# Performance work log

Measured on AMD Instinct MI355X. Metric: run time of the kernel, lower is better.

The kernel has to match this reference:

```python
import jax, jax.numpy as jnp
import numpy as np
from jax import lax

B, T_HIST, T_PRED = 8192, 11, 80
IN, H = 2, 64


def _glorot(key, shape, fan):
    bound = 1.0 / np.sqrt(fan)
    return jax.random.uniform(key, shape, jnp.float32, -bound, bound)


def setup_inputs() -> dict:
    key = jax.random.key(0)
    ks = jax.random.split(key, 20)
    inp = {"x": jax.random.normal(ks[0], (B, T_HIST, IN), jnp.float32)}
    # encoder / decoder: 2-layer tanh RNN, PyTorch param layout (out_features first)
    for pfx, base in (("enc", 1), ("dec", 9)):
        inp[f"{pfx}_Wih0"] = _glorot(ks[base + 0], (H, IN), H)
        inp[f"{pfx}_Whh0"] = _glorot(ks[base + 1], (H, H), H)
        inp[f"{pfx}_bih0"] = _glorot(ks[base + 2], (H,), H)
        inp[f"{pfx}_bhh0"] = _glorot(ks[base + 3], (H,), H)
        inp[f"{pfx}_Wih1"] = _glorot(ks[base + 4], (H, H), H)
        inp[f"{pfx}_Whh1"] = _glorot(ks[base + 5], (H, H), H)
        inp[f"{pfx}_bih1"] = _glorot(ks[base + 6], (H,), H)
        inp[f"{pfx}_bhh1"] = _glorot(ks[base + 7], (H,), H)
    inp["fc_W"] = _glorot(ks[17], (2, H), H)
    inp["fc_b"] = _glorot(ks[18], (2,), H)
    return inp


def _rnn_layer(x_seq, h0, Wih, Whh, bih, bhh):
    # x_seq: [T, B, in]; tanh RNN cell, returns (h_T, all hidden states [T, B, H])
    def step(h, x_t):
        h_new = jnp.tanh(x_t @ Wih.T + bih + h @ Whh.T + bhh)
        return h_new, h_new
    return lax.scan(step, h0, x_seq)


def reference(x,
              enc_Wih0, enc_Whh0, enc_bih0, enc_bhh0,
              enc_Wih1, enc_Whh1, enc_bih1, enc_bhh1,
              dec_Wih0, dec_Whh0, dec_bih0, dec_bhh0,
              dec_Wih1, dec_Whh1, dec_bih1, dec_bhh1,
              fc_W, fc_b):
    b = x.shape[0]
    h0 = jnp.zeros((b, H), x.dtype)
    x_seq = jnp.swapaxes(x, 0, 1)  # [T, B, 2]
    # encoder (dropout inactive in eval)
    h1_T, hs0 = _rnn_layer(x_seq, h0, enc_Wih0, enc_Whh0, enc_bih0, enc_bhh0)
    h2_T, _ = _rnn_layer(hs0, h0, enc_Wih1, enc_Whh1, enc_bih1, enc_bhh1)

    def dec_step(carry, _):
        h1, h2, inp = carry
        h1 = jnp.tanh(inp @ dec_Wih0.T + dec_bih0 + h1 @ dec_Whh0.T + dec_bhh0)
        h2 = jnp.tanh(h1 @ dec_Wih1.T + dec_bih1 + h2 @ dec_Whh1.T + dec_bhh1)
        pred = h2 @ fc_W.T + fc_b  # [B, 2]
        return (h1, h2, pred), pred

    init = (h1_T, h2_T, x[:, -1, :])
    _, preds = lax.scan(dec_step, init, None, length=T_PRED)  # [80, B, 2]
    return jnp.swapaxes(preds, 0, 1)  # [B, 80, 2]
```

## Files before the change

### kernel.cpp

```cpp
#include <hip/hip_runtime.h>

typedef __attribute__((ext_vector_type(8))) _Float16 f16x8;
typedef __attribute__((ext_vector_type(4))) float   f32x4;

namespace {
constexpr int kB    = 8192;
constexpr int kTH   = 11;
constexpr int kTP   = 80;
constexpr int kM    = 16;
constexpr int kStrH = 72;
}

__device__ __forceinline__ f16x8 cvt8(const float* f) {
    f16x8 v;
#pragma unroll
    for (int j = 0; j < 8; ++j) v[j] = (_Float16)f[j];
    return v;
}

__device__ __forceinline__ void loadB1(const float* __restrict__ W, int col, int q,
                                       f16x8 (&Bf)[2]) {
#pragma unroll
    for (int c = 0; c < 2; ++c) {
        const float* src = W + col * 64 + c * 32 + q * 8;
        const float4 a = reinterpret_cast<const float4*>(src)[0];
        const float4 b = reinterpret_cast<const float4*>(src)[1];
        float f[8] = {a.x, a.y, a.z, a.w, b.x, b.y, b.z, b.w};
        Bf[c] = cvt8(f);
    }
}

__device__ __forceinline__ void loadBfc(const float* __restrict__ fcW, int p, int q,
                                        f16x8 (&Bf)[2]) {
#pragma unroll
    for (int c = 0; c < 2; ++c) {
        float f[8];
#pragma unroll
        for (int j = 0; j < 8; ++j)
            f[j] = (p < 2) ? fcW[p * 64 + c * 32 + q * 8 + j] : 0.f;
        Bf[c] = cvt8(f);
    }
}

__device__ __forceinline__ void loadBG(const float* __restrict__ fcW, float w0, float w1,
                                       int q, f16x8 (&Bf)[2]) {
#pragma unroll
    for (int c = 0; c < 2; ++c) {
        float f[8];
#pragma unroll
        for (int j = 0; j < 8; ++j) {
            const int k = c * 32 + q * 8 + j;
            f[j] = w0 * fcW[k] + w1 * fcW[64 + k];
        }
        Bf[c] = cvt8(f);
    }
}

__device__ __forceinline__ f16x8 read_frag(const _Float16* plane, int off) {
    return *reinterpret_cast<const f16x8*>(plane + off);
}

__device__ __forceinline__ f32x4 mfma1(f16x8 a, f16x8 b, f32x4 acc) {
    return __builtin_amdgcn_mfma_f32_16x16x32_f16(a, b, acc, 0, 0, 0);
}

__device__ __forceinline__ float fast_tanh(float x) {
    const float e = __builtin_amdgcn_exp2f(x * 2.8853900817779268f);
    return fmaf(-2.0f, __builtin_amdgcn_rcpf(e + 1.0f), 1.0f);
}

__global__ __attribute__((amdgpu_waves_per_eu(2, 2))) __launch_bounds__(256)
void traj_rnn_kernel(
    const float* __restrict__ x,
    const float* __restrict__ eWih0, const float* __restrict__ eWhh0,
    const float* __restrict__ ebih0, const float* __restrict__ ebhh0,
    const float* __restrict__ eWih1, const float* __restrict__ eWhh1,
    const float* __restrict__ ebih1, const float* __restrict__ ebhh1,
    const float* __restrict__ dWih0, const float* __restrict__ dWhh0,
    const float* __restrict__ dbih0, const float* __restrict__ dbhh0,
    const float* __restrict__ dWih1, const float* __restrict__ dWhh1,
    const float* __restrict__ dbih1, const float* __restrict__ dbhh1,
    const float* __restrict__ fcW, const float* __restrict__ fcb,
    float* __restrict__ out)
{
    const int tid  = threadIdx.x;
    const int wv   = tid >> 6;
    const int lane = tid & 63;
    const int p    = lane & 15;
    const int q    = lane >> 4;
    const int col  = wv * 16 + p;
    const int r0   = blockIdx.x * kM;

    __shared__ __align__(16) _Float16 Hhi1[kM * kStrH];
    __shared__ __align__(16) _Float16 Hhi2[kM * kStrH];
    __shared__ __align__(16) float xbuf[kM * kTH * 2];
    __shared__ __align__(16) float predbuf[kM * kTP * 2];

    for (int i = tid; i < kM * kTH * 2; i += 256)
        xbuf[i] = x[r0 * (kTH * 2) + i];

    f16x8 H1f[2], H2f[2];
#pragma unroll
    for (int c = 0; c < 2; ++c) {
        H1f[c] = f16x8{0, 0, 0, 0, 0, 0, 0, 0};
        H2f[c] = f16x8{0, 0, 0, 0, 0, 0, 0, 0};
    }
    __syncthreads();

    const int aoff = p * kStrH;

    {
        const float b0 = ebih0[col] + ebhh0[col];
        const float b1 = ebih1[col] + ebhh1[col];
        const float w0 = eWih0[col * 2 + 0];
        const float w1 = eWih0[col * 2 + 1];
        f16x8 B0[2], B1[2], B2[2];
        loadB1(eWhh0, col, q, B0);
        loadB1(eWih1, col, q, B1);
        loadB1(eWhh1, col, q, B2);

        f32x4 P1 = {b0, b0, b0, b0};

#pragma unroll 1
        for (int t = 0; t < kTH; ++t) {
#pragma unroll
            for (int r = 0; r < 4; ++r) {
                const float2 xv = *reinterpret_cast<const float2*>(
                    &xbuf[(4 * q + r) * (kTH * 2) + 2 * t]);
                const float h1 = fast_tanh(fmaf(w0, xv.x, fmaf(w1, xv.y, P1[r])));
                Hhi1[(4 * q + r) * kStrH + col] = (_Float16)h1;
            }
            f32x4 a2 = {b1, b1, b1, b1};
#pragma unroll
            for (int c = 0; c < 2; ++c)
                a2 = mfma1(H2f[c], B2[c], a2);
            __syncthreads();

#pragma unroll
            for (int c = 0; c < 2; ++c)
                H1f[c] = read_frag(Hhi1, aoff + c * 32 + q * 8);
#pragma unroll
            for (int c = 0; c < 2; ++c)
                a2 = mfma1(H1f[c], B1[c], a2);
#pragma unroll
            for (int r = 0; r < 4; ++r) {
                const float h2 = fast_tanh(a2[r]);
                Hhi2[(4 * q + r) * kStrH + col] = (_Float16)h2;
            }
            __syncthreads();

#pragma unroll
            for (int c = 0; c < 2; ++c)
                H2f[c] = read_frag(Hhi2, aoff + c * 32 + q * 8);
            f32x4 np = {b0, b0, b0, b0};
#pragma unroll
            for (int c = 0; c < 2; ++c)
                np = mfma1(H1f[c], B0[c], np);
            P1 = np;
        }
    }

    {
        const float b0 = dbih0[col] + dbhh0[col];
        const float b1 = dbih1[col] + dbhh1[col];
        const float w0 = dWih0[col * 2 + 0];
        const float w1 = dWih0[col * 2 + 1];
        const float fb0 = fcb[0];
        const float fb1 = fcb[1];
        const float b0p = b0 + w0 * fb0 + w1 * fb1;
        const float fbp = (p == 0) ? fb0 : fb1;
        f16x8 B0[2], B1[2], B2[2], BF[2], BG[2];
        loadB1(dWhh0, col, q, B0);
        loadB1(dWih1, col, q, B1);
        loadB1(dWhh1, col, q, B2);
        loadBfc(fcW, p, q, BF);
        loadBG(fcW, w0, w1, q, BG);

        f32x4 P1 = {b0, b0, b0, b0};
#pragma unroll
        for (int c = 0; c < 2; ++c)
            P1 = mfma1(H1f[c], B0[c], P1);
#pragma unroll
        for (int r = 0; r < 4; ++r) {
            const float2 xv = *reinterpret_cast<const float2*>(
                &xbuf[(4 * q + r) * (kTH * 2) + 2 * (kTH - 1)]);
            P1[r] = fmaf(w0, xv.x, fmaf(w1, xv.y, P1[r]));
        }

#pragma unroll 2
        for (int t = 0; t < kTP; ++t) {
#pragma unroll
            for (int r = 0; r < 4; ++r) {
                const float h1 = fast_tanh(P1[r]);
                Hhi1[(4 * q + r) * kStrH + col] = (_Float16)h1;
            }
            f32x4 a2 = {b1, b1, b1, b1};
#pragma unroll
            for (int c = 0; c < 2; ++c)
                a2 = mfma1(H2f[c], B2[c], a2);
            __syncthreads();

#pragma unroll
            for (int c = 0; c < 2; ++c)
                H1f[c] = read_frag(Hhi1, aoff + c * 32 + q * 8);
#pragma unroll
            for (int c = 0; c < 2; ++c)
                a2 = mfma1(H1f[c], B1[c], a2);
#pragma unroll
            for (int r = 0; r < 4; ++r) {
                const float h2 = fast_tanh(a2[r]);
                Hhi2[(4 * q + r) * kStrH + col] = (_Float16)h2;
            }
            __syncthreads();

#pragma unroll
            for (int c = 0; c < 2; ++c)
                H2f[c] = read_frag(Hhi2, aoff + c * 32 + q * 8);
            f32x4 ng = {b0p, b0p, b0p, b0p};
            f32x4 nb = {0.f, 0.f, 0.f, 0.f};
#pragma unroll
            for (int c = 0; c < 2; ++c) {
                ng = mfma1(H2f[c], BG[c], ng);
                nb = mfma1(H1f[c], B0[c], nb);
            }
            P1 = ng + nb;

            f32x4 fcC = {0.f, 0.f, 0.f, 0.f};
#pragma unroll
            for (int c = 0; c < 2; ++c)
                fcC = mfma1(H2f[c], BF[c], fcC);
            if (wv == 0 && p < 2) {
#pragma unroll
                for (int r = 0; r < 4; ++r)
                    predbuf[((4 * q + r) * kTP + t) * 2 + p] = fcC[r] + fbp;
            }
        }
    }

    __syncthreads();
    {
        float4* dst = reinterpret_cast<float4*>(out + r0 * (kTP * 2));
        const float4* src = reinterpret_cast<const float4*>(predbuf);
        for (int i = tid; i < kM * kTP * 2 / 4; i += 256)
            dst[i] = src[i];
    }
}

extern "C" void kernel_launch(void* const* d_in, const int* in_sizes, int n_in,
                              void* d_out, int out_size, void* d_ws, size_t ws_size,
                              hipStream_t stream) {
    const float* x     = (const float*)d_in[0];
    const float* eWih0 = (const float*)d_in[1];
    const float* eWhh0 = (const float*)d_in[2];
    const float* ebih0 = (const float*)d_in[3];
    const float* ebhh0 = (const float*)d_in[4];
    const float* eWih1 = (const float*)d_in[5];
    const float* eWhh1 = (const float*)d_in[6];
    const float* ebih1 = (const float*)d_in[7];
    const float* ebhh1 = (const float*)d_in[8];
    const float* dWih0 = (const float*)d_in[9];
    const float* dWhh0 = (const float*)d_in[10];
    const float* dbih0 = (const float*)d_in[11];
    const float* dbhh0 = (const float*)d_in[12];
    const float* dWih1 = (const float*)d_in[13];
    const float* dWhh1 = (const float*)d_in[14];
    const float* dbih1 = (const float*)d_in[15];
    const float* dbhh1 = (const float*)d_in[16];
    const float* fcW   = (const float*)d_in[17];
    const float* fcb   = (const float*)d_in[18];
    float* out = (float*)d_out;

    dim3 grid(kB / kM);
    dim3 block(256);
    traj_rnn_kernel<<<grid, block, 0, stream>>>(
        x, eWih0, eWhh0, ebih0, ebhh0, eWih1, eWhh1, ebih1, ebhh1,
        dWih0, dWhh0, dbih0, dbhh0, dWih1, dWhh1, dbih1, dbhh1,
        fcW, fcb, out);
}
```

Measured before the change: 141.0 us.

## Ping-pong two 16-row groups per block to overlap recurrence phases

Each block now handles 32 rows in two groups of four waves. The groups run alternate halves of each RNN step (layer-1 phase vs layer-2 phase) between shared barriers, so one group's MFMA/tanh work fills the other's barrier wait. Weights for encoder and decoder are preloaded upfront, and the grid is halved with 512-thread blocks. This raises register pressure (both weight sets live) and couples the groups through block-wide barriers.

```diff
diff --git a/kernel.cpp b/kernel.cpp
--- a/kernel.cpp
+++ b/kernel.cpp
@@ -69,7 +69,7 @@
     return fmaf(-2.0f, __builtin_amdgcn_rcpf(e + 1.0f), 1.0f);
 }
 
-__global__ __attribute__((amdgpu_waves_per_eu(2, 2))) __launch_bounds__(256)
+__global__ __attribute__((amdgpu_waves_per_eu(2, 2))) __launch_bounds__(512)
 void traj_rnn_kernel(
     const float* __restrict__ x,
     const float* __restrict__ eWih0, const float* __restrict__ eWhh0,
@@ -84,164 +84,191 @@
     float* __restrict__ out)
 {
     const int tid  = threadIdx.x;
-    const int wv   = tid >> 6;
+    const int grp  = tid >> 8;
+    const int wvg  = (tid >> 6) & 3;
     const int lane = tid & 63;
     const int p    = lane & 15;
     const int q    = lane >> 4;
-    const int col  = wv * 16 + p;
-    const int r0   = blockIdx.x * kM;
-
-    __shared__ __align__(16) _Float16 Hhi1[kM * kStrH];
-    __shared__ __align__(16) _Float16 Hhi2[kM * kStrH];
-    __shared__ __align__(16) float xbuf[kM * kTH * 2];
-    __shared__ __align__(16) float predbuf[kM * kTP * 2];
-
-    for (int i = tid; i < kM * kTH * 2; i += 256)
-        xbuf[i] = x[r0 * (kTH * 2) + i];
-
-    f16x8 H1f[2], H2f[2];
-#pragma unroll
-    for (int c = 0; c < 2; ++c) {
-        H1f[c] = f16x8{0, 0, 0, 0, 0, 0, 0, 0};
-        H2f[c] = f16x8{0, 0, 0, 0, 0, 0, 0, 0};
-    }
-    __syncthreads();
-
+    const int col  = wvg * 16 + p;
+
+    __shared__ __align__(16) _Float16 H1s[2][kM * kStrH];
+    __shared__ __align__(16) _Float16 H2s[2][kM * kStrH];
+    __shared__ __align__(16) float xbuf[2][kM * kTH * 2];
+    __shared__ __align__(16) float predbuf[2][kM * kTP * 2];
+
+    for (int i = tid; i < 2 * kM * kTH * 2; i += 512)
+        (&xbuf[0][0])[i] = x[blockIdx.x * 32 * (kTH * 2) + i];
+
+    _Float16* h1p = H1s[grp];
+    _Float16* h2p = H2s[grp];
+    const float* xb = xbuf[grp];
+    float*       pb = predbuf[grp];
+
+    const f16x8 Z = {0, 0, 0, 0, 0, 0, 0, 0};
+    f16x8 H1f0 = Z, H1f1 = Z, H2f0 = Z, H2f1 = Z;
     const int aoff = p * kStrH;
 
-    {
-        const float b0 = ebih0[col] + ebhh0[col];
-        const float b1 = ebih1[col] + ebhh1[col];
-        const float w0 = eWih0[col * 2 + 0];
-        const float w1 = eWih0[col * 2 + 1];
-        f16x8 B0[2], B1[2], B2[2];
-        loadB1(eWhh0, col, q, B0);
-        loadB1(eWih1, col, q, B1);
-        loadB1(eWhh1, col, q, B2);
-
-        f32x4 P1 = {b0, b0, b0, b0};
-
-#pragma unroll 1
-        for (int t = 0; t < kTH; ++t) {
-#pragma unroll
-            for (int r = 0; r < 4; ++r) {
-                const float2 xv = *reinterpret_cast<const float2*>(
-                    &xbuf[(4 * q + r) * (kTH * 2) + 2 * t]);
-                const float h1 = fast_tanh(fmaf(w0, xv.x, fmaf(w1, xv.y, P1[r])));
-                Hhi1[(4 * q + r) * kStrH + col] = (_Float16)h1;
-            }
-            f32x4 a2 = {b1, b1, b1, b1};
-#pragma unroll
-            for (int c = 0; c < 2; ++c)
-                a2 = mfma1(H2f[c], B2[c], a2);
-            __syncthreads();
-
-#pragma unroll
-            for (int c = 0; c < 2; ++c)
-                H1f[c] = read_frag(Hhi1, aoff + c * 32 + q * 8);
-#pragma unroll
-            for (int c = 0; c < 2; ++c)
-                a2 = mfma1(H1f[c], B1[c], a2);
-#pragma unroll
-            for (int r = 0; r < 4; ++r) {
-                const float h2 = fast_tanh(a2[r]);
-                Hhi2[(4 * q + r) * kStrH + col] = (_Float16)h2;
-            }
-            __syncthreads();
-
-#pragma unroll
-            for (int c = 0; c < 2; ++c)
-                H2f[c] = read_frag(Hhi2, aoff + c * 32 + q * 8);
-            f32x4 np = {b0, b0, b0, b0};
-#pragma unroll
-            for (int c = 0; c < 2; ++c)
-                np = mfma1(H1f[c], B0[c], np);
-            P1 = np;
-        }
-    }
-
-    {
-        const float b0 = dbih0[col] + dbhh0[col];
-        const float b1 = dbih1[col] + dbhh1[col];
-        const float w0 = dWih0[col * 2 + 0];
-        const float w1 = dWih0[col * 2 + 1];
-        const float fb0 = fcb[0];
-        const float fb1 = fcb[1];
-        const float b0p = b0 + w0 * fb0 + w1 * fb1;
-        const float fbp = (p == 0) ? fb0 : fb1;
-        f16x8 B0[2], B1[2], B2[2], BF[2], BG[2];
-        loadB1(dWhh0, col, q, B0);
-        loadB1(dWih1, col, q, B1);
-        loadB1(dWhh1, col, q, B2);
-        loadBfc(fcW, p, q, BF);
-        loadBG(fcW, w0, w1, q, BG);
-
-        f32x4 P1 = {b0, b0, b0, b0};
-#pragma unroll
-        for (int c = 0; c < 2; ++c)
-            P1 = mfma1(H1f[c], B0[c], P1);
+    const float b0e = ebih0[col] + ebhh0[col];
+    const float b1e = ebih1[col] + ebhh1[col];
+    const float w0e = eWih0[col * 2 + 0];
+    const float w1e = eWih0[col * 2 + 1];
+    f16x8 B0e[2], B1e[2], B2e[2];
+    loadB1(eWhh0, col, q, B0e);
+    loadB1(eWih1, col, q, B1e);
+    loadB1(eWhh1, col, q, B2e);
+
+    const float b0d = dbih0[col] + dbhh0[col];
+    const float b1d = dbih1[col] + dbhh1[col];
+    const float w0d = dWih0[col * 2 + 0];
+    const float w1d = dWih0[col * 2 + 1];
+    const float fb0 = fcb[0];
+    const float fb1 = fcb[1];
+    const float b0p = b0d + w0d * fb0 + w1d * fb1;
+    const float fbp = (p == 0) ? fb0 : fb1;
+    f16x8 B0d[2], B1d[2], B2d[2], BG[2], BF[2];
+    loadB1(dWhh0, col, q, B0d);
+    loadB1(dWih1, col, q, B1d);
+    loadB1(dWhh1, col, q, B2d);
+    loadBG(fcW, w0d, w1d, q, BG);
+    loadBfc(fcW, p, q, BF);
+
+    f32x4 P1 = {b0e, b0e, b0e, b0e};
+    f32x4 a2 = {0.f, 0.f, 0.f, 0.f};
+    f32x4 nb = {0.f, 0.f, 0.f, 0.f};
+
+    __syncthreads();
+
+    auto A_enc = [&](int t) {
+        if (t > 0) {
+            H2f0 = read_frag(h2p, aoff + q * 8);
+            H2f1 = read_frag(h2p, aoff + 32 + q * 8);
+        }
 #pragma unroll
         for (int r = 0; r < 4; ++r) {
             const float2 xv = *reinterpret_cast<const float2*>(
-                &xbuf[(4 * q + r) * (kTH * 2) + 2 * (kTH - 1)]);
-            P1[r] = fmaf(w0, xv.x, fmaf(w1, xv.y, P1[r]));
-        }
-
-#pragma unroll 2
-        for (int t = 0; t < kTP; ++t) {
-#pragma unroll
-            for (int r = 0; r < 4; ++r) {
-                const float h1 = fast_tanh(P1[r]);
-                Hhi1[(4 * q + r) * kStrH + col] = (_Float16)h1;
-            }
-            f32x4 a2 = {b1, b1, b1, b1};
-#pragma unroll
-            for (int c = 0; c < 2; ++c)
-                a2 = mfma1(H2f[c], B2[c], a2);
-            __syncthreads();
-
-#pragma unroll
-            for (int c = 0; c < 2; ++c)
-                H1f[c] = read_frag(Hhi1, aoff + c * 32 + q * 8);
-#pragma unroll
-            for (int c = 0; c < 2; ++c)
-                a2 = mfma1(H1f[c], B1[c], a2);
-#pragma unroll
-            for (int r = 0; r < 4; ++r) {
-                const float h2 = fast_tanh(a2[r]);
-                Hhi2[(4 * q + r) * kStrH + col] = (_Float16)h2;
-            }
-            __syncthreads();
-
-#pragma unroll
-            for (int c = 0; c < 2; ++c)
-                H2f[c] = read_frag(Hhi2, aoff + c * 32 + q * 8);
-            f32x4 ng = {b0p, b0p, b0p, b0p};
-            f32x4 nb = {0.f, 0.f, 0.f, 0.f};
-#pragma unroll
-            for (int c = 0; c < 2; ++c) {
-                ng = mfma1(H2f[c], BG[c], ng);
-                nb = mfma1(H1f[c], B0[c], nb);
-            }
-            P1 = ng + nb;
-
-            f32x4 fcC = {0.f, 0.f, 0.f, 0.f};
-#pragma unroll
-            for (int c = 0; c < 2; ++c)
-                fcC = mfma1(H2f[c], BF[c], fcC);
-            if (wv == 0 && p < 2) {
-#pragma unroll
-                for (int r = 0; r < 4; ++r)
-                    predbuf[((4 * q + r) * kTP + t) * 2 + p] = fcC[r] + fbp;
-            }
-        }
-    }
-
-    __syncthreads();
+                &xb[(4 * q + r) * (kTH * 2) + 2 * t]);
+            const float h1 = fast_tanh(fmaf(w0e, xv.x, fmaf(w1e, xv.y, P1[r])));
+            h1p[(4 * q + r) * kStrH + col] = (_Float16)h1;
+        }
+        a2 = f32x4{b1e, b1e, b1e, b1e};
+        a2 = mfma1(H2f0, B2e[0], a2);
+        a2 = mfma1(H2f1, B2e[1], a2);
+    };
+    auto B_enc = [&](int t) {
+        (void)t;
+        H1f0 = read_frag(h1p, aoff + q * 8);
+        H1f1 = read_frag(h1p, aoff + 32 + q * 8);
+        a2 = mfma1(H1f0, B1e[0], a2);
+        a2 = mfma1(H1f1, B1e[1], a2);
+#pragma unroll
+        for (int r = 0; r < 4; ++r) {
+            const float h2 = fast_tanh(a2[r]);
+            h2p[(4 * q + r) * kStrH + col] = (_Float16)h2;
+        }
+        f32x4 np = {b0e, b0e, b0e, b0e};
+        np = mfma1(H1f0, B0e[0], np);
+        np = mfma1(H1f1, B0e[1], np);
+        P1 = np;
+    };
+    auto A_dec0 = [&]() {
+        H2f0 = read_frag(h2p, aoff + q * 8);
+        H2f1 = read_frag(h2p, aoff + 32 + q * 8);
+        P1 = f32x4{b0d, b0d, b0d, b0d};
+        P1 = mfma1(H1f0, B0d[0], P1);
+        P1 = mfma1(H1f1, B0d[1], P1);
+#pragma unroll
+        for (int r = 0; r < 4; ++r) {
+            const float2 xv = *reinterpret_cast<const float2*>(
+                &xb[(4 * q + r) * (kTH * 2) + 2 * (kTH - 1)]);
+            P1[r] = fmaf(w0d, xv.x, fmaf(w1d, xv.y, P1[r]));
+        }
+#pragma unroll
+        for (int r = 0; r < 4; ++r)
+            h1p[(4 * q + r) * kStrH + col] = (_Float16)fast_tanh(P1[r]);
+        a2 = f32x4{b1d, b1d, b1d, b1d};
+        a2 = mfma1(H2f0, B2d[0], a2);
+        a2 = mfma1(H2f1, B2d[1], a2);
+    };
+    auto A_dec = [&](int t) {
+        H2f0 = read_frag(h2p, aoff + q * 8);
+        H2f1 = read_frag(h2p, aoff + 32 + q * 8);
+        f32x4 ng = {b0p, b0p, b0p, b0p};
+        ng = mfma1(H2f0, BG[0], ng);
+        ng = mfma1(H2f1, BG[1], ng);
+        P1 = ng + nb;
+        f32x4 fcC = {0.f, 0.f, 0.f, 0.f};
+        fcC = mfma1(H2f0, BF[0], fcC);
+        fcC = mfma1(H2f1, BF[1], fcC);
+        if (wvg == 0 && p < 2) {
+#pragma unroll
+            for (int r = 0; r < 4; ++r)
+                pb[((4 * q + r) * kTP + (t - 1)) * 2 + p] = fcC[r] + fbp;
+        }
+#pragma unroll
+        for (int r = 0; r < 4; ++r)
+            h1p[(4 * q + r) * kStrH + col] = (_Float16)fast_tanh(P1[r]);
+        a2 = f32x4{b1d, b1d, b1d, b1d};
+        a2 = mfma1(H2f0, B2d[0], a2);
+        a2 = mfma1(H2f1, B2d[1], a2);
+    };
+    auto B_dec = [&](int t) {
+        (void)t;
+        H1f0 = read_frag(h1p, aoff + q * 8);
+        H1f1 = read_frag(h1p, aoff + 32 + q * 8);
+        a2 = mfma1(H1f0, B1d[0], a2);
+        a2 = mfma1(H1f1, B1d[1], a2);
+#pragma unroll
+        for (int r = 0; r < 4; ++r) {
+            const float h2 = fast_tanh(a2[r]);
+            h2p[(4 * q + r) * kStrH + col] = (_Float16)h2;
+        }
+        nb = f32x4{0.f, 0.f, 0.f, 0.f};
+        nb = mfma1(H1f0, B0d[0], nb);
+        nb = mfma1(H1f1, B0d[1], nb);
+    };
+    auto FC_ep = [&]() {
+        H2f0 = read_frag(h2p, aoff + q * 8);
+        H2f1 = read_frag(h2p, aoff + 32 + q * 8);
+        f32x4 fcC = {0.f, 0.f, 0.f, 0.f};
+        fcC = mfma1(H2f0, BF[0], fcC);
+        fcC = mfma1(H2f1, BF[1], fcC);
+        if (wvg == 0 && p < 2) {
+#pragma unroll
+            for (int r = 0; r < 4; ++r)
+                pb[((4 * q + r) * kTP + (kTP - 1)) * 2 + p] = fcC[r] + fbp;
+        }
+    };
+
+    if (grp == 0) A_enc(0);
+    __syncthreads();
+#pragma unroll 1
+    for (int k = 0; ; ++k) {
+        if (grp == 0) B_enc(k); else A_enc(k);
+        __syncthreads();
+        if (k == kTH - 1) break;
+        if (grp == 0) A_enc(k + 1); else B_enc(k);
+        __syncthreads();
+    }
+    if (grp == 0) A_dec0(); else B_enc(kTH - 1);
+    __syncthreads();
+    if (grp == 0) B_dec(0); else A_dec0();
+    __syncthreads();
+#pragma unroll 1
+    for (int k = 0; k < kTP - 1; ++k) {
+        if (grp == 0) A_dec(k + 1); else B_dec(k);
+        __syncthreads();
+        if (grp == 0) B_dec(k + 1); else A_dec(k + 1);
+        __syncthreads();
+    }
+    if (grp == 0) FC_ep(); else B_dec(kTP - 1);
+    __syncthreads();
+    if (grp != 0) FC_ep();
+    __syncthreads();
+
     {
-        float4* dst = reinterpret_cast<float4*>(out + r0 * (kTP * 2));
-        const float4* src = reinterpret_cast<const float4*>(predbuf);
-        for (int i = tid; i < kM * kTP * 2 / 4; i += 256)
+        float4* dst = reinterpret_cast<float4*>(out + blockIdx.x * 32 * (kTP * 2));
+        const float4* src = reinterpret_cast<const float4*>(&predbuf[0][0]);
+        for (int i = tid; i < 2 * kM * kTP * 2 / 4; i += 512)
             dst[i] = src[i];
     }
 }
@@ -270,8 +297,8 @@
     const float* fcb   = (const float*)d_in[18];
     float* out = (float*)d_out;
 
-    dim3 grid(kB / kM);
-    dim3 block(256);
+    dim3 grid(kB / 32);
+    dim3 block(512);
     traj_rnn_kernel<<<grid, block, 0, stream>>>(
         x, eWih0, eWhh0, ebih0, ebhh0, eWih1, eWhh1, ebih1, ebhh1,
         dWih0, dWhh0, dbih0, dbhh0, dWih1, dWhh1, dbih1, dbhh1,
```

Result: slower. 149.2 us (+5.8%).

## Compute layer-2 redundantly per wave to halve barriers per RNN step

Applied to the files above, without the earlier changes.

Each wave now computes the full 64-wide layer-2 hidden state itself and stages it in a private shared-memory slice, so it no longer needs a block-wide barrier before the next step. The layer-1 hidden state is double-buffered in shared memory, leaving one __syncthreads per timestep instead of two. The encoder-to-decoder handoff is software-pipelined by shifting the layer-2 and fc work one step behind layer 1. The cost is four times the layer-2 MFMA and tanh work per wave, and many more weight fragments held in registers, which may lower occupancy.

```diff
diff --git a/kernel.cpp b/kernel.cpp
--- a/kernel.cpp
+++ b/kernel.cpp
@@ -4,11 +4,11 @@
 typedef __attribute__((ext_vector_type(4))) float   f32x4;
 
 namespace {
-constexpr int kB    = 8192;
-constexpr int kTH   = 11;
-constexpr int kTP   = 80;
-constexpr int kM    = 16;
-constexpr int kStrH = 72;
+constexpr int kB   = 8192;
+constexpr int kTH  = 11;
+constexpr int kTP  = 80;
+constexpr int kM   = 16;
+constexpr int kStr = 72;
 }
 
 __device__ __forceinline__ f16x8 cvt8(const float* f) {
@@ -91,149 +91,183 @@
     const int col  = wv * 16 + p;
     const int r0   = blockIdx.x * kM;
 
-    __shared__ __align__(16) _Float16 Hhi1[kM * kStrH];
-    __shared__ __align__(16) _Float16 Hhi2[kM * kStrH];
+    __shared__ __align__(16) _Float16 h1sh[2][kM * kStr];
+    __shared__ __align__(16) _Float16 h2pr[4][kM * kStr];
     __shared__ __align__(16) float xbuf[kM * kTH * 2];
     __shared__ __align__(16) float predbuf[kM * kTP * 2];
 
     for (int i = tid; i < kM * kTH * 2; i += 256)
         xbuf[i] = x[r0 * (kTH * 2) + i];
 
-    f16x8 H1f[2], H2f[2];
-#pragma unroll
-    for (int c = 0; c < 2; ++c) {
-        H1f[c] = f16x8{0, 0, 0, 0, 0, 0, 0, 0};
-        H2f[c] = f16x8{0, 0, 0, 0, 0, 0, 0, 0};
-    }
+    _Float16* h2w  = h2pr[wv];
+    const int aoff = p * kStr;
+
+    const f16x8 Z = {0, 0, 0, 0, 0, 0, 0, 0};
+    f16x8 H1f0 = Z, H1f1 = Z;
+    f16x8 h2A0 = Z, h2A1 = Z;
+    f32x4 a2p[4];
+
+    const float b0e = ebih0[col] + ebhh0[col];
+    const float w0e = eWih0[col * 2 + 0], w1e = eWih0[col * 2 + 1];
+    float b1e4[4];
+    f16x8 B0e[2], B1e[8], B2e[8];
+    loadB1(eWhh0, col, q, B0e);
+    {
+        f16x8 tmp[2];
+#pragma unroll
+        for (int n = 0; n < 4; ++n) {
+            const int cn = p + 16 * n;
+            b1e4[n] = ebih1[cn] + ebhh1[cn];
+            loadB1(eWih1, cn, q, tmp); B1e[2 * n] = tmp[0]; B1e[2 * n + 1] = tmp[1];
+            loadB1(eWhh1, cn, q, tmp); B2e[2 * n] = tmp[0]; B2e[2 * n + 1] = tmp[1];
+        }
+    }
+
     __syncthreads();
 
-    const int aoff = p * kStrH;
-
-    {
-        const float b0 = ebih0[col] + ebhh0[col];
-        const float b1 = ebih1[col] + ebhh1[col];
-        const float w0 = eWih0[col * 2 + 0];
-        const float w1 = eWih0[col * 2 + 1];
-        f16x8 B0[2], B1[2], B2[2];
-        loadB1(eWhh0, col, q, B0);
-        loadB1(eWih1, col, q, B1);
-        loadB1(eWhh1, col, q, B2);
-
-        f32x4 P1 = {b0, b0, b0, b0};
+    auto h2_step = [&](const f16x8* B1x) {
+        f32x4 a0 = a2p[0], a1 = a2p[1], a2 = a2p[2], a3 = a2p[3];
+        a0 = mfma1(H1f0, B1x[0], a0);  a1 = mfma1(H1f0, B1x[2], a1);
+        a2 = mfma1(H1f0, B1x[4], a2);  a3 = mfma1(H1f0, B1x[6], a3);
+        a0 = mfma1(H1f1, B1x[1], a0);  a1 = mfma1(H1f1, B1x[3], a1);
+        a2 = mfma1(H1f1, B1x[5], a2);  a3 = mfma1(H1f1, B1x[7], a3);
+#pragma unroll
+        for (int r = 0; r < 4; ++r) {
+            h2w[(4 * q + r) * kStr + p +  0] = (_Float16)fast_tanh(a0[r]);
+            h2w[(4 * q + r) * kStr + p + 16] = (_Float16)fast_tanh(a1[r]);
+            h2w[(4 * q + r) * kStr + p + 32] = (_Float16)fast_tanh(a2[r]);
+            h2w[(4 * q + r) * kStr + p + 48] = (_Float16)fast_tanh(a3[r]);
+        }
+        h2A0 = read_frag(h2w, aoff + q * 8);
+        h2A1 = read_frag(h2w, aoff + 32 + q * 8);
+    };
+    auto a2p_next = [&](const f16x8* B2x, const float* b1x) {
+#pragma unroll
+        for (int n = 0; n < 4; ++n) {
+            f32x4 v = {b1x[n], b1x[n], b1x[n], b1x[n]};
+            v = mfma1(h2A0, B2x[2 * n], v);
+            v = mfma1(h2A1, B2x[2 * n + 1], v);
+            a2p[n] = v;
+        }
+    };
+
+    {
+#pragma unroll
+        for (int r = 0; r < 4; ++r) {
+            const float2 xv = *reinterpret_cast<const float2*>(
+                &xbuf[(4 * q + r) * (kTH * 2) + 0]);
+            h1sh[0][(4 * q + r) * kStr + col] =
+                (_Float16)fast_tanh(fmaf(w0e, xv.x, fmaf(w1e, xv.y, b0e)));
+        }
+#pragma unroll
+        for (int n = 0; n < 4; ++n)
+            a2p[n] = f32x4{b1e4[n], b1e4[n], b1e4[n], b1e4[n]};
+        __syncthreads();
+    }
 
 #pragma unroll 1
-        for (int t = 0; t < kTH; ++t) {
-#pragma unroll
-            for (int r = 0; r < 4; ++r) {
-                const float2 xv = *reinterpret_cast<const float2*>(
-                    &xbuf[(4 * q + r) * (kTH * 2) + 2 * t]);
-                const float h1 = fast_tanh(fmaf(w0, xv.x, fmaf(w1, xv.y, P1[r])));
-                Hhi1[(4 * q + r) * kStrH + col] = (_Float16)h1;
-            }
-            f32x4 a2 = {b1, b1, b1, b1};
-#pragma unroll
-            for (int c = 0; c < 2; ++c)
-                a2 = mfma1(H2f[c], B2[c], a2);
-            __syncthreads();
-
-#pragma unroll
-            for (int c = 0; c < 2; ++c)
-                H1f[c] = read_frag(Hhi1, aoff + c * 32 + q * 8);
-#pragma unroll
-            for (int c = 0; c < 2; ++c)
-                a2 = mfma1(H1f[c], B1[c], a2);
-#pragma unroll
-            for (int r = 0; r < 4; ++r) {
-                const float h2 = fast_tanh(a2[r]);
-                Hhi2[(4 * q + r) * kStrH + col] = (_Float16)h2;
-            }
-            __syncthreads();
-
-#pragma unroll
-            for (int c = 0; c < 2; ++c)
-                H2f[c] = read_frag(Hhi2, aoff + c * 32 + q * 8);
-            f32x4 np = {b0, b0, b0, b0};
-#pragma unroll
-            for (int c = 0; c < 2; ++c)
-                np = mfma1(H1f[c], B0[c], np);
-            P1 = np;
-        }
-    }
-
-    {
-        const float b0 = dbih0[col] + dbhh0[col];
-        const float b1 = dbih1[col] + dbhh1[col];
-        const float w0 = dWih0[col * 2 + 0];
-        const float w1 = dWih0[col * 2 + 1];
-        const float fb0 = fcb[0];
-        const float fb1 = fcb[1];
-        const float b0p = b0 + w0 * fb0 + w1 * fb1;
-        const float fbp = (p == 0) ? fb0 : fb1;
-        f16x8 B0[2], B1[2], B2[2], BF[2], BG[2];
-        loadB1(dWhh0, col, q, B0);
-        loadB1(dWih1, col, q, B1);
-        loadB1(dWhh1, col, q, B2);
-        loadBfc(fcW, p, q, BF);
-        loadBG(fcW, w0, w1, q, BG);
-
-        f32x4 P1 = {b0, b0, b0, b0};
-#pragma unroll
-        for (int c = 0; c < 2; ++c)
-            P1 = mfma1(H1f[c], B0[c], P1);
+    for (int t = 1; t < kTH; ++t) {
+        const _Float16* rpl = h1sh[(t - 1) & 1];
+        _Float16*       wpl = h1sh[t & 1];
+        H1f0 = read_frag(rpl, aoff + q * 8);
+        H1f1 = read_frag(rpl, aoff + 32 + q * 8);
+        f32x4 np = {b0e, b0e, b0e, b0e};
+        np = mfma1(H1f0, B0e[0], np);
+        np = mfma1(H1f1, B0e[1], np);
+#pragma unroll
+        for (int r = 0; r < 4; ++r) {
+            const float2 xv = *reinterpret_cast<const float2*>(
+                &xbuf[(4 * q + r) * (kTH * 2) + 2 * t]);
+            wpl[(4 * q + r) * kStr + col] =
+                (_Float16)fast_tanh(fmaf(w0e, xv.x, fmaf(w1e, xv.y, np[r])));
+        }
+        h2_step(B1e);
+        a2p_next(B2e, b1e4);
+        __syncthreads();
+    }
+
+    const float b0d = dbih0[col] + dbhh0[col];
+    const float w0d = dWih0[col * 2 + 0], w1d = dWih0[col * 2 + 1];
+    const float fb0 = fcb[0], fb1 = fcb[1];
+    const float b0p = b0d + w0d * fb0 + w1d * fb1;
+    const float fbp = (p == 0) ? fb0 : fb1;
+    float b1d4[4];
+    f16x8 B0d[2], BG[2], BF[2], B1d[8], B2d[8];
+    loadB1(dWhh0, col, q, B0d);
+    loadBG(fcW, w0d, w1d, q, BG);
+    loadBfc(fcW, p, q, BF);
+    {
+        f16x8 tmp[2];
+#pragma unroll
+        for (int n = 0; n < 4; ++n) {
+            const int cn = p + 16 * n;
+            b1d4[n] = dbih1[cn] + dbhh1[cn];
+            loadB1(dWih1, cn, q, tmp); B1d[2 * n] = tmp[0]; B1d[2 * n + 1] = tmp[1];
+            loadB1(dWhh1, cn, q, tmp); B2d[2 * n] = tmp[0]; B2d[2 * n + 1] = tmp[1];
+        }
+    }
+
+    {
+        const _Float16* rpl = h1sh[0];
+        _Float16*       wpl = h1sh[1];
+        H1f0 = read_frag(rpl, aoff + q * 8);
+        H1f1 = read_frag(rpl, aoff + 32 + q * 8);
+        f32x4 np = {b0d, b0d, b0d, b0d};
+        np = mfma1(H1f0, B0d[0], np);
+        np = mfma1(H1f1, B0d[1], np);
 #pragma unroll
         for (int r = 0; r < 4; ++r) {
             const float2 xv = *reinterpret_cast<const float2*>(
                 &xbuf[(4 * q + r) * (kTH * 2) + 2 * (kTH - 1)]);
-            P1[r] = fmaf(w0, xv.x, fmaf(w1, xv.y, P1[r]));
-        }
-
-#pragma unroll 2
-        for (int t = 0; t < kTP; ++t) {
-#pragma unroll
-            for (int r = 0; r < 4; ++r) {
-                const float h1 = fast_tanh(P1[r]);
-                Hhi1[(4 * q + r) * kStrH + col] = (_Float16)h1;
-            }
-            f32x4 a2 = {b1, b1, b1, b1};
-#pragma unroll
-            for (int c = 0; c < 2; ++c)
-                a2 = mfma1(H2f[c], B2[c], a2);
-            __syncthreads();
-
-#pragma unroll
-            for (int c = 0; c < 2; ++c)
-                H1f[c] = read_frag(Hhi1, aoff + c * 32 + q * 8);
-#pragma unroll
-            for (int c = 0; c < 2; ++c)
-                a2 = mfma1(H1f[c], B1[c], a2);
-#pragma unroll
-            for (int r = 0; r < 4; ++r) {
-                const float h2 = fast_tanh(a2[r]);
-                Hhi2[(4 * q + r) * kStrH + col] = (_Float16)h2;
-            }
-            __syncthreads();
-
-#pragma unroll
-            for (int c = 0; c < 2; ++c)
-                H2f[c] = read_frag(Hhi2, aoff + c * 32 + q * 8);
-            f32x4 ng = {b0p, b0p, b0p, b0p};
-            f32x4 nb = {0.f, 0.f, 0.f, 0.f};
-#pragma unroll
-            for (int c = 0; c < 2; ++c) {
-                ng = mfma1(H2f[c], BG[c], ng);
-                nb = mfma1(H1f[c], B0[c], nb);
-            }
-            P1 = ng + nb;
-
-            f32x4 fcC = {0.f, 0.f, 0.f, 0.f};
-#pragma unroll
-            for (int c = 0; c < 2; ++c)
-                fcC = mfma1(H2f[c], BF[c], fcC);
-            if (wv == 0 && p < 2) {
-#pragma unroll
-                for (int r = 0; r < 4; ++r)
-                    predbuf[((4 * q + r) * kTP + t) * 2 + p] = fcC[r] + fbp;
-            }
+            wpl[(4 * q + r) * kStr + col] =
+                (_Float16)fast_tanh(fmaf(w0d, xv.x, fmaf(w1d, xv.y, np[r])));
+        }
+        h2_step(B1e);
+        a2p_next(B2d, b1d4);
+        __syncthreads();
+    }
+
+#pragma unroll 1
+    for (int d = 1; d < kTP; ++d) {
+        const _Float16* rpl = h1sh[d & 1];
+        _Float16*       wpl = h1sh[(d & 1) ^ 1];
+        H1f0 = read_frag(rpl, aoff + q * 8);
+        H1f1 = read_frag(rpl, aoff + 32 + q * 8);
+        f32x4 nb = {0.f, 0.f, 0.f, 0.f};
+        nb = mfma1(H1f0, B0d[0], nb);
+        nb = mfma1(H1f1, B0d[1], nb);
+        h2_step(B1d);
+        f32x4 ng = {b0p, b0p, b0p, b0p};
+        ng = mfma1(h2A0, BG[0], ng);
+        ng = mfma1(h2A1, BG[1], ng);
+        f32x4 P = ng + nb;
+#pragma unroll
+        for (int r = 0; r < 4; ++r)
+            wpl[(4 * q + r) * kStr + col] = (_Float16)fast_tanh(P[r]);
+        f32x4 fcC = {0.f, 0.f, 0.f, 0.f};
+        fcC = mfma1(h2A0, BF[0], fcC);
+        fcC = mfma1(h2A1, BF[1], fcC);
+        if (wv == 0 && p < 2) {
+#pragma unroll
+            for (int r = 0; r < 4; ++r)
+                predbuf[((4 * q + r) * kTP + (d - 1)) * 2 + p] = fcC[r] + fbp;
+        }
+        a2p_next(B2d, b1d4);
+        __syncthreads();
+    }
+
+    {
+        const _Float16* rpl = h1sh[kTP & 1];
+        H1f0 = read_frag(rpl, aoff + q * 8);
+        H1f1 = read_frag(rpl, aoff + 32 + q * 8);
+        h2_step(B1d);
+        f32x4 fcC = {0.f, 0.f, 0.f, 0.f};
+        fcC = mfma1(h2A0, BF[0], fcC);
+        fcC = mfma1(h2A1, BF[1], fcC);
+        if (wv == 0 && p < 2) {
+#pragma unroll
+            for (int r = 0; r < 4; ++r)
+                predbuf[((4 * q + r) * kTP + (kTP - 1)) * 2 + p] = fcC[r] + fbp;
         }
     }
 
```

Result: slower. 190.8 us (+35.3%).
